# Optimization experiments

Hardware: AMD Instinct MI355X
Metric: run time of the kernel (lower is better)

Reference implementation:

```python
import jax, jax.numpy as jnp
import numpy as np

D_MODEL = 1024
NUM_HEADS = 16
D_K = D_MODEL // NUM_HEADS
THETA = 10000.0
SEQ = 4096
BATCH = 1


def _rope(x, token_positions):
    # x: [b, h, s, d_k]; interleaved even/odd rotation as in the torch module
    kd = jnp.arange(0, D_K, 2, dtype=jnp.float32) / D_K          # [d_k/2]
    angles = token_positions[:, None].astype(jnp.float32) / (THETA ** kd)  # [s, d_k/2]
    cos_pos = jnp.cos(angles)
    sin_pos = jnp.sin(angles)
    x_even = x[..., 0::2]
    x_odd = x[..., 1::2]
    rot_even = x_even * cos_pos - x_odd * sin_pos
    rot_odd = x_even * sin_pos + x_odd * cos_pos
    rot = jnp.stack([rot_even, rot_odd], axis=-1)                # [..., d_k/2, 2]
    return rot.reshape(*x.shape[:-1], D_K)


def setup_inputs() -> dict:
    key = jax.random.key(0)
    k1, k2, k3 = jax.random.split(key, 3)
    std_qkv = np.sqrt(2.0 / (D_MODEL + 3 * D_MODEL))
    std_o = np.sqrt(2.0 / (D_MODEL + D_MODEL))
    x = jax.random.normal(k1, (BATCH, SEQ, D_MODEL), dtype=jnp.float32)
    Wqkv = jax.random.normal(k2, (3 * D_MODEL, D_MODEL), dtype=jnp.float32) * std_qkv
    Wo = jax.random.normal(k3, (D_MODEL, D_MODEL), dtype=jnp.float32) * std_o
    token_positions = jnp.arange(SEQ, dtype=jnp.int32)
    return {"x": x, "Wqkv": Wqkv, "Wo": Wo, "token_positions": token_positions}


def reference(x, Wqkv, Wo, token_positions):
    b, s, _ = x.shape
    qkv = jnp.einsum('bsd,ed->bse', x, Wqkv)                      # [b, s, 3*d_model]
    q, k, v = jnp.split(qkv, 3, axis=-1)

    def to_heads(t):
        return t.reshape(b, s, NUM_HEADS, D_K).transpose(0, 2, 1, 3)  # [b, h, s, d_k]

    q, k, v = to_heads(q), to_heads(k), to_heads(v)
    q = _rope(q, token_positions)
    k = _rope(k, token_positions)

    scores = jnp.einsum('bhqd,bhkd->bhqk', q, k) / jnp.sqrt(jnp.float32(D_K))
    mask = jnp.tril(jnp.ones((s, s), dtype=bool))
    scores = jnp.where(mask, scores, -jnp.inf)
    attn = jax.nn.softmax(scores, axis=-1)
    out = jnp.einsum('bhqk,bhkd->bhqd', attn, v)                  # [b, h, s, d_k]
    out = out.transpose(0, 2, 1, 3).reshape(b, s, D_MODEL)
    return jnp.einsum('bsd,ed->bse', out, Wo)
```

## Files before the change

kernel.cpp:

```cpp
#include <hip/hip_runtime.h>
#include <cstdint>

typedef unsigned short u16;
typedef __attribute__((ext_vector_type(8))) short short8;
typedef __attribute__((ext_vector_type(4))) float float4v;

__device__ __forceinline__ float bf2f(u16 u) {
    union { unsigned int i; float f; } v; v.i = ((unsigned int)u) << 16; return v.f;
}
__device__ __forceinline__ u16 f2bf(float f) {
    union { float f; unsigned int i; } v; v.f = f;
    unsigned int i = v.i;
    i += 0x7fffu + ((i >> 16) & 1u);
    return (u16)(i >> 16);
}
__device__ __forceinline__ unsigned cvt_pk_bf16(float lo, float hi) {
    unsigned r;
    asm("v_cvt_pk_bf16_f32 %0, %1, %2" : "=v"(r) : "v"(lo), "v"(hi));
    return r;
}
__device__ __forceinline__ void gl2lds16(const u16* g, u16* l) {
    __builtin_amdgcn_global_load_lds((const __attribute__((address_space(1))) void*)g,
                                     (__attribute__((address_space(3))) void*)l, 16, 0, 0);
}
__device__ __forceinline__ uint4 cvt8(const float* __restrict__ p) {
    float4 a = *(const float4*)p;
    float4 b = *(const float4*)(p + 4);
    u16 t[8] = {f2bf(a.x), f2bf(a.y), f2bf(a.z), f2bf(a.w),
                f2bf(b.x), f2bf(b.y), f2bf(b.z), f2bf(b.w)};
    return *(const uint4*)t;
}

__global__ void cvt_f32_bf16(const float* __restrict__ src, u16* __restrict__ dst, int n8) {
    int i = blockIdx.x * blockDim.x + threadIdx.x;
    if (i >= n8) return;
    *(uint4*)(dst + (size_t)i * 8) = cvt8(src + (size_t)i * 8);
}

__global__ void zero_f32(float* __restrict__ p, int n4) {
    int i = blockIdx.x * blockDim.x + threadIdx.x;
    if (i >= n4) return;
    float4 z = {0.f, 0.f, 0.f, 0.f};
    *(float4*)(p + (size_t)i * 4) = z;
}

__global__ __launch_bounds__(256) void gemm_bt(const u16* __restrict__ A,
                                               const u16* __restrict__ B,
                                               u16* __restrict__ C,
                                               int M, int N, int K) {
    __shared__ u16 As[128 * 32];
    __shared__ u16 Bs[128 * 32];
    const int tid  = threadIdx.x;
    const int wave = tid >> 6, lane = tid & 63;
    const int lg = lane >> 4, lr = lane & 15;
    const int bm = blockIdx.x * 128, bn = blockIdx.y * 128;
    const int wm = (wave & 1) * 64, wn = (wave >> 1) * 64;
    const int row = tid >> 2, co = (tid & 3) * 8;

    float4v acc[4][4] = {};

    for (int k0 = 0; k0 < K; k0 += 32) {
        gl2lds16(A + (size_t)(bm + row) * K + k0 + co,      As + tid * 8);
        gl2lds16(A + (size_t)(bm + 64 + row) * K + k0 + co, As + (tid + 256) * 8);
        gl2lds16(B + (size_t)(bn + row) * K + k0 + co,      Bs + tid * 8);
        gl2lds16(B + (size_t)(bn + 64 + row) * K + k0 + co, Bs + (tid + 256) * 8);
        __syncthreads();

        short8 af[4], bf[4];
        #pragma unroll
        for (int i = 0; i < 4; ++i)
            af[i] = *(const short8*)(As + (wm + i * 16 + lr) * 32 + lg * 8);
        #pragma unroll
        for (int j = 0; j < 4; ++j)
            bf[j] = *(const short8*)(Bs + (wn + j * 16 + lr) * 32 + lg * 8);
        #pragma unroll
        for (int i = 0; i < 4; ++i)
            #pragma unroll
            for (int j = 0; j < 4; ++j)
                acc[i][j] = __builtin_amdgcn_mfma_f32_16x16x32_bf16(af[i], bf[j], acc[i][j], 0, 0, 0);
        __syncthreads();
    }

    #pragma unroll
    for (int i = 0; i < 4; ++i)
        #pragma unroll
        for (int j = 0; j < 4; ++j)
            #pragma unroll
            for (int r = 0; r < 4; ++r) {
                int rw = bm + wm + i * 16 + lg * 4 + r;
                int cl = bn + wn + j * 16 + lr;
                C[(size_t)rw * N + cl] = f2bf(acc[i][j][r]);
            }
}

__global__ void rope_kernel(u16* __restrict__ qkv, const int* __restrict__ pos, int S) {
    int idx = blockIdx.x * blockDim.x + threadIdx.x;
    int s = idx >> 10;
    if (s >= S) return;
    int p    = idx & 1023;
    int part = p >> 9;
    int wi   = p & 511;
    int head = wi >> 5;
    int i    = wi & 31;
    int col  = part * 1024 + head * 64 + 2 * i;

    u16* ptr = qkv + (size_t)s * 3072 + col;
    ushort2 v = *(const ushort2*)ptr;
    float xe = bf2f(v.x), xo = bf2f(v.y);
    float freq = __expf(-(float)i * 0.2878231366242557f);
    float ang  = (float)pos[s] * freq;
    float sn = sinf(ang), cs = cosf(ang);
    float re = xe * cs - xo * sn;
    float ro = xe * sn + xo * cs;
    if (part == 0) { re *= 0.18033688011112042f; ro *= 0.18033688011112042f; }
    ushort2 o; o.x = f2bf(re); o.y = f2bf(ro);
    *(ushort2*)ptr = o;
}

__global__ __launch_bounds__(256) void transpose_v(const u16* __restrict__ qkv,
                                                   u16* __restrict__ VT) {
    __shared__ u16 T[64 * 65];
    const int h = blockIdx.y, s0 = blockIdx.x * 64;
    const int tid = threadIdx.x;
    #pragma unroll
    for (int i = 0; i < 2; ++i) {
        int seg = i * 256 + tid;
        int r = seg >> 3, c8 = (seg & 7) * 8;
        u16 tmp[8];
        *(uint4*)tmp = *(const uint4*)(qkv + (size_t)(s0 + r) * 3072 + 2048 + h * 64 + c8);
        #pragma unroll
        for (int j = 0; j < 8; ++j) T[r * 65 + c8 + j] = tmp[j];
    }
    __syncthreads();
    #pragma unroll
    for (int i = 0; i < 2; ++i) {
        int seg = i * 256 + tid;
        int d = seg >> 3, s8 = (seg & 7) * 8;
        u16 tmp[8];
        #pragma unroll
        for (int j = 0; j < 8; ++j) tmp[j] = T[(s8 + j) * 65 + d];
        *(uint4*)(VT + (size_t)(h * 64 + d) * 4096 + s0 + s8) = *(const uint4*)tmp;
    }
}

__device__ __forceinline__ void attn_tile(const u16* __restrict__ Ksub,
                                          const u16* __restrict__ Vsub,
                                          u16* __restrict__ Psw,
                                          int tbase, int qrow0, int q_abs,
                                          int lg, int lr, int swz,
                                          const short8 qf[2], float4v o_acc[4], float& rs) {
    float4v sc[4];
    #pragma unroll
    for (int jt = 0; jt < 4; ++jt) {
        float4v a = {};
        #pragma unroll
        for (int kk = 0; kk < 2; ++kk) {
            short8 kf = *(const short8*)(Ksub + (jt * 16 + lr) * 64 + (((kk * 4 + lg) ^ swz) * 8));
            a = __builtin_amdgcn_mfma_f32_16x16x32_bf16(kf, qf[kk], a, 0, 0, 0);
        }
        sc[jt] = a;
    }
    const bool mk = (tbase + 63 > qrow0);
    #pragma unroll
    for (int jt = 0; jt < 4; ++jt) {
        float e[4];
        #pragma unroll
        for (int r = 0; r < 4; ++r) {
            float s = sc[jt][r];
            if (mk && (tbase + jt * 16 + lg * 4 + r > q_abs)) s = -30000.f;
            e[r] = __builtin_amdgcn_exp2f(fminf(s, 86.562f));
        }
        rs += (e[0] + e[1]) + (e[2] + e[3]);
        uint2 w;
        w.x = cvt_pk_bf16(e[0], e[1]);
        w.y = cvt_pk_bf16(e[2], e[3]);
        *(uint2*)(Psw + lr * 72 + jt * 16 + lg * 4) = w;
    }
    short8 pf[2];
    #pragma unroll
    for (int kk = 0; kk < 2; ++kk)
        pf[kk] = *(const short8*)(Psw + lr * 72 + kk * 32 + lg * 8);
    #pragma unroll
    for (int jd = 0; jd < 4; ++jd) {
        float4v a = o_acc[jd];
        #pragma unroll
        for (int kk = 0; kk < 2; ++kk) {
            short8 vf = *(const short8*)(Vsub + (jd * 16 + lr) * 64 + (((kk * 4 + lg) ^ swz) * 8));
            a = __builtin_amdgcn_mfma_f32_16x16x32_bf16(pf[kk], vf, a, 0, 0, 0);
        }
        o_acc[jd] = a;
    }
}

__global__ __launch_bounds__(512) void attn_kernel(const u16* __restrict__ qkv,
                                                   const u16* __restrict__ VT,
                                                   float* __restrict__ acc,
                                                   float* __restrict__ lac) {
    __shared__ u16 Ks[2 * 64 * 64];
    __shared__ u16 Vt[2 * 64 * 64];
    __shared__ u16 Ps[8][16 * 72];

    const int tid  = threadIdx.x;
    const int wave = tid >> 6, lane = tid & 63;
    const int lg = lane >> 4, lr = lane & 15;
    const int h  = blockIdx.y;
    const int z  = blockIdx.z;

    const int srow = tid >> 3;
    const int sg   = tid & 7;
    const int sco  = sg * 8;
    const int sldso = srow * 64 + ((sg ^ (srow & 7)) * 8);
    const int swz = (lr & 7);

    const u16* Kgbase = qkv + (size_t)srow * 3072 + 1024 + h * 64 + sco;
    const u16* Vgbase = VT + (size_t)(h * 64 + srow) * 4096 + sco;

    #pragma unroll 1
    for (int part = 0; part < 2; ++part) {
        const int qt = part ? (31 - (int)blockIdx.x) : (int)blockIdx.x;
        const int qb = qt * 128;
        const int qrow0 = qb + wave * 16;
        const int q_abs = qrow0 + lr;
        const int tmax = qb + 64;
        const int t0s  = z * 64;

        short8 qf[2];
        #pragma unroll
        for (int kk = 0; kk < 2; ++kk)
            qf[kk] = *(const short8*)(qkv + (size_t)(qrow0 + lr) * 3072 + h * 64 + kk * 32 + lg * 8);

        float4v o_acc[4] = {};
        float rs = 0.f;

        uint4 rK0 = *(const uint4*)(Kgbase + (size_t)t0s * 3072);
        uint4 rV0 = *(const uint4*)(Vgbase + t0s);
        const bool pB = (t0s + 128 <= tmax);
        uint4 rK1, rV1;
        if (pB) {
            rK1 = *(const uint4*)(Kgbase + (size_t)(t0s + 128) * 3072);
            rV1 = *(const uint4*)(Vgbase + t0s + 128);
        }
        __syncthreads();
        *(uint4*)(Ks + sldso) = rK0;
        *(uint4*)(Vt + sldso) = rV0;
        if (pB) {
            *(uint4*)(Ks + 4096 + sldso) = rK1;
            *(uint4*)(Vt + 4096 + sldso) = rV1;
        }
        __syncthreads();

        for (int t0 = t0s; t0 <= tmax; t0 += 256) {
            const bool hasB  = (t0 + 128 <= tmax);
            const bool hasN  = (t0 + 256 <= tmax);
            const bool hasNB = (t0 + 384 <= tmax);
            if (hasN) {
                rK0 = *(const uint4*)(Kgbase + (size_t)(t0 + 256) * 3072);
                rV0 = *(const uint4*)(Vgbase + t0 + 256);
            }
            if (hasNB) {
                rK1 = *(const uint4*)(Kgbase + (size_t)(t0 + 384) * 3072);
                rV1 = *(const uint4*)(Vgbase + t0 + 384);
            }

            attn_tile(Ks, Vt, Ps[wave], t0, qrow0, q_abs, lg, lr, swz, qf, o_acc, rs);
            if (hasB)
                attn_tile(Ks + 4096, Vt + 4096, Ps[wave], t0 + 128, qrow0, q_abs,
                          lg, lr, swz, qf, o_acc, rs);

            if (hasN) {
                __syncthreads();
                *(uint4*)(Ks + sldso) = rK0;
                *(uint4*)(Vt + sldso) = rV0;
                if (hasNB) {
                    *(uint4*)(Ks + 4096 + sldso) = rK1;
                    *(uint4*)(Vt + 4096 + sldso) = rV1;
                }
                __syncthreads();
            }
        }

        float t = rs;
        t += __shfl_xor(t, 16, 64);
        t += __shfl_xor(t, 32, 64);
        if (lane < 16)
            atomicAdd(&lac[(size_t)(qrow0 + lr) * 16 + h], t);

        #pragma unroll
        for (int jd = 0; jd < 4; ++jd)
            #pragma unroll
            for (int r = 0; r < 4; ++r) {
                int s = qrow0 + lg * 4 + r;
                int d = jd * 16 + lr;
                atomicAdd(&acc[(size_t)s * 1024 + h * 64 + d], o_acc[jd][r]);
            }
    }
}

__global__ void norm_o(const float* __restrict__ acc, const float* __restrict__ lac,
                       u16* __restrict__ qkv) {
    int i = blockIdx.x * blockDim.x + threadIdx.x;
    if (i >= 4096 * 1024 / 8) return;
    int e0 = i * 8;
    int s = e0 >> 10, c = e0 & 1023, h = c >> 6;
    float inv = 1.0f / lac[(size_t)s * 16 + h];
    float4 a = *(const float4*)(acc + e0);
    float4 b = *(const float4*)(acc + e0 + 4);
    u16 t[8] = {f2bf(a.x * inv), f2bf(a.y * inv), f2bf(a.z * inv), f2bf(a.w * inv),
                f2bf(b.x * inv), f2bf(b.y * inv), f2bf(b.z * inv), f2bf(b.w * inv)};
    *(uint4*)(qkv + (size_t)s * 3072 + c) = *(const uint4*)t;
}

__global__ __launch_bounds__(256) void gemm_oproj(const u16* __restrict__ A,
                                                  const u16* __restrict__ B,
                                                  float* __restrict__ C) {
    __shared__ u16 As[128 * 32];
    __shared__ u16 Bs[128 * 32];
    const int tid  = threadIdx.x;
    const int wave = tid >> 6, lane = tid & 63;
    const int lg = lane >> 4, lr = lane & 15;
    const int bm = blockIdx.x * 128, bn = blockIdx.y * 128;
    const int wm = (wave & 1) * 64, wn = (wave >> 1) * 64;
    const int row = tid >> 2, co = (tid & 3) * 8;

    float4v acc[4][4] = {};

    for (int k0 = 0; k0 < 1024; k0 += 32) {
        gl2lds16(A + (size_t)(bm + row) * 3072 + k0 + co,      As + tid * 8);
        gl2lds16(A + (size_t)(bm + 64 + row) * 3072 + k0 + co, As + (tid + 256) * 8);
        gl2lds16(B + (size_t)(bn + row) * 1024 + k0 + co,      Bs + tid * 8);
        gl2lds16(B + (size_t)(bn + 64 + row) * 1024 + k0 + co, Bs + (tid + 256) * 8);
        __syncthreads();

        short8 af[4], bf[4];
        #pragma unroll
        for (int i = 0; i < 4; ++i)
            af[i] = *(const short8*)(As + (wm + i * 16 + lr) * 32 + lg * 8);
        #pragma unroll
        for (int j = 0; j < 4; ++j)
            bf[j] = *(const short8*)(Bs + (wn + j * 16 + lr) * 32 + lg * 8);
        #pragma unroll
        for (int i = 0; i < 4; ++i)
            #pragma unroll
            for (int j = 0; j < 4; ++j)
                acc[i][j] = __builtin_amdgcn_mfma_f32_16x16x32_bf16(af[i], bf[j], acc[i][j], 0, 0, 0);
        __syncthreads();
    }

    #pragma unroll
    for (int i = 0; i < 4; ++i)
        #pragma unroll
        for (int j = 0; j < 4; ++j)
            #pragma unroll
            for (int r = 0; r < 4; ++r) {
                int rw = bm + wm + i * 16 + lg * 4 + r;
                int cl = bn + wn + j * 16 + lr;
                C[(size_t)rw * 1024 + cl] = acc[i][j][r];
            }
}

__global__ void fill_diag(float* __restrict__ p, size_t n, float mark) {
    size_t i = (size_t)blockIdx.x * blockDim.x + threadIdx.x;
    if (i < n) p[i] = 0.f;
    if (i == 0) p[0] = mark;
}

extern "C" void kernel_launch(void* const* d_in, const int* in_sizes, int n_in,
                              void* d_out, int out_size, void* d_ws, size_t ws_size,
                              hipStream_t stream) {
    int ix = -1, iwq = -1, iwo = -1, ip = -1;
    for (int i = 0; i < n_in; ++i) {
        if      (in_sizes[i] == 4096 * 1024) ix = i;
        else if (in_sizes[i] == 3072 * 1024) iwq = i;
        else if (in_sizes[i] == 1024 * 1024) iwo = i;
        else if (in_sizes[i] == 4096)        ip = i;
    }
    float* out = (float*)d_out;
    const size_t OUT_E = (size_t)4096 * 1024;
    const size_t QKV_E = (size_t)4096 * 3072;
    const size_t NEED  = QKV_E * 2 + (size_t)3072 * 1024 * 2;

    if (ix < 0 || iwq < 0 || iwo < 0 || ip < 0 || out_size != (int)OUT_E) {
        fill_diag<<<(int)((OUT_E + 255) / 256), 256, 0, stream>>>(out, OUT_E, 1000.0f);
        return;
    }
    if (ws_size < NEED) {
        fill_diag<<<(int)((OUT_E + 255) / 256), 256, 0, stream>>>(out, OUT_E, 500.0f);
        return;
    }
    const float* x    = (const float*)d_in[ix];
    const float* Wqkv = (const float*)d_in[iwq];
    const float* Wo   = (const float*)d_in[iwo];
    const int*   pos  = (const int*)d_in[ip];

    u16* qkv   = (u16*)d_ws;
    u16* wq_bf = (u16*)d_ws + QKV_E;
    u16* wo_bf = wq_bf;
    float* lac = (float*)((char*)wq_bf + 2 * 1024 * 1024 + 65536);
    u16* x_bf  = (u16*)d_out;
    u16* VT    = (u16*)d_out + OUT_E;
    float* acc = (float*)d_in[ix];

    cvt_f32_bf16<<<2048, 256, 0, stream>>>(x, x_bf, 4096 * 1024 / 8);
    cvt_f32_bf16<<<1536, 256, 0, stream>>>(Wqkv, wq_bf, 3072 * 1024 / 8);
    gemm_bt<<<dim3(32, 24), 256, 0, stream>>>(x_bf, wq_bf, qkv, 4096, 3072, 1024);
    zero_f32<<<4096, 256, 0, stream>>>(acc, 4096 * 1024 / 4);
    zero_f32<<<16, 256, 0, stream>>>(lac, 4096 * 16 / 4);
    cvt_f32_bf16<<<512, 256, 0, stream>>>(Wo, wo_bf, 1024 * 1024 / 8);
    rope_kernel<<<16384, 256, 0, stream>>>(qkv, pos, 4096);
    transpose_v<<<dim3(64, 16), 256, 0, stream>>>(qkv, VT);
    attn_kernel<<<dim3(16, 16, 2), 512, 0, stream>>>(qkv, VT, acc, lac);
    norm_o<<<2048, 256, 0, stream>>>(acc, lac, qkv);
    gemm_oproj<<<dim3(32, 8), 256, 0, stream>>>(qkv, wo_bf, out);
}
```

Measured before the change: 245.7 us.

## Fuse RoPE into QKV GEMM epilogue, merge prep kernels, split attention KV three ways

Applies RoPE and the Q scaling inside the QKV GEMM epilogue, exchanging the even/odd partner with a lane shuffle, which removes a separate read-modify-write pass over Q and K. The converts and zero-fills are merged into two kernels to reduce launch count. Attention now splits the key range across three z-slices (stride 384, second tile at +192) instead of two, raising block count, and the P scratch row pitch changes from 72 to 80 to alter the LDS bank pattern. This adds per-element sincos work in the GEMM epilogue and relies on the atomic-style accumulation handling a third partial.

```diff
diff --git a/kernel.cpp b/kernel.cpp
--- a/kernel.cpp
+++ b/kernel.cpp
@@ -31,23 +31,35 @@
     return *(const uint4*)t;
 }
 
-__global__ void cvt_f32_bf16(const float* __restrict__ src, u16* __restrict__ dst, int n8) {
+__global__ void cvt_xw(const float* __restrict__ x, const float* __restrict__ wq,
+                       u16* __restrict__ xb, u16* __restrict__ wqb) {
     int i = blockIdx.x * blockDim.x + threadIdx.x;
-    if (i >= n8) return;
-    *(uint4*)(dst + (size_t)i * 8) = cvt8(src + (size_t)i * 8);
-}
-
-__global__ void zero_f32(float* __restrict__ p, int n4) {
+    if (i < 524288) {
+        *(uint4*)(xb + (size_t)i * 8) = cvt8(x + (size_t)i * 8);
+    } else {
+        int j = i - 524288;
+        *(uint4*)(wqb + (size_t)j * 8) = cvt8(wq + (size_t)j * 8);
+    }
+}
+
+__global__ void zero_cvt(float* __restrict__ acc, float* __restrict__ lac,
+                         const float* __restrict__ wo, u16* __restrict__ wob) {
     int i = blockIdx.x * blockDim.x + threadIdx.x;
-    if (i >= n4) return;
     float4 z = {0.f, 0.f, 0.f, 0.f};
-    *(float4*)(p + (size_t)i * 4) = z;
-}
-
-__global__ __launch_bounds__(256) void gemm_bt(const u16* __restrict__ A,
-                                               const u16* __restrict__ B,
-                                               u16* __restrict__ C,
-                                               int M, int N, int K) {
+    if (i < 1048576) {
+        *(float4*)(acc + (size_t)i * 4) = z;
+    } else if (i < 1064960) {
+        *(float4*)(lac + (size_t)(i - 1048576) * 4) = z;
+    } else {
+        int j = i - 1064960;
+        *(uint4*)(wob + (size_t)j * 8) = cvt8(wo + (size_t)j * 8);
+    }
+}
+
+__global__ __launch_bounds__(256) void gemm_qkv(const u16* __restrict__ A,
+                                                const u16* __restrict__ B,
+                                                u16* __restrict__ C,
+                                                const int* __restrict__ pos) {
     __shared__ u16 As[128 * 32];
     __shared__ u16 Bs[128 * 32];
     const int tid  = threadIdx.x;
@@ -59,11 +71,11 @@
 
     float4v acc[4][4] = {};
 
-    for (int k0 = 0; k0 < K; k0 += 32) {
-        gl2lds16(A + (size_t)(bm + row) * K + k0 + co,      As + tid * 8);
-        gl2lds16(A + (size_t)(bm + 64 + row) * K + k0 + co, As + (tid + 256) * 8);
-        gl2lds16(B + (size_t)(bn + row) * K + k0 + co,      Bs + tid * 8);
-        gl2lds16(B + (size_t)(bn + 64 + row) * K + k0 + co, Bs + (tid + 256) * 8);
+    for (int k0 = 0; k0 < 1024; k0 += 32) {
+        gl2lds16(A + (size_t)(bm + row) * 1024 + k0 + co,      As + tid * 8);
+        gl2lds16(A + (size_t)(bm + 64 + row) * 1024 + k0 + co, As + (tid + 256) * 8);
+        gl2lds16(B + (size_t)(bn + row) * 1024 + k0 + co,      Bs + tid * 8);
+        gl2lds16(B + (size_t)(bn + 64 + row) * 1024 + k0 + co, Bs + (tid + 256) * 8);
         __syncthreads();
 
         short8 af[4], bf[4];
@@ -81,40 +93,35 @@
         __syncthreads();
     }
 
+    const int colbase = bn + wn;
+    const bool dorope = colbase < 2048;
+    const float qsc = (colbase < 1024) ? 0.18033688011112042f : 1.0f;
+    float freqs[4];
+    if (dorope) {
+        #pragma unroll
+        for (int j = 0; j < 4; ++j)
+            freqs[j] = __expf(-(float)((j * 16 + lr) >> 1) * 0.2878231366242557f);
+    }
     #pragma unroll
     for (int i = 0; i < 4; ++i)
         #pragma unroll
-        for (int j = 0; j < 4; ++j)
+        for (int r = 0; r < 4; ++r) {
+            const int rw = bm + wm + i * 16 + lg * 4 + r;
+            const float pr = dorope ? (float)pos[rw] : 0.f;
             #pragma unroll
-            for (int r = 0; r < 4; ++r) {
-                int rw = bm + wm + i * 16 + lg * 4 + r;
-                int cl = bn + wn + j * 16 + lr;
-                C[(size_t)rw * N + cl] = f2bf(acc[i][j][r]);
-            }
-}
-
-__global__ void rope_kernel(u16* __restrict__ qkv, const int* __restrict__ pos, int S) {
-    int idx = blockIdx.x * blockDim.x + threadIdx.x;
-    int s = idx >> 10;
-    if (s >= S) return;
-    int p    = idx & 1023;
-    int part = p >> 9;
-    int wi   = p & 511;
-    int head = wi >> 5;
-    int i    = wi & 31;
-    int col  = part * 1024 + head * 64 + 2 * i;
-
-    u16* ptr = qkv + (size_t)s * 3072 + col;
-    ushort2 v = *(const ushort2*)ptr;
-    float xe = bf2f(v.x), xo = bf2f(v.y);
-    float freq = __expf(-(float)i * 0.2878231366242557f);
-    float ang  = (float)pos[s] * freq;
-    float sn = sinf(ang), cs = cosf(ang);
-    float re = xe * cs - xo * sn;
-    float ro = xe * sn + xo * cs;
-    if (part == 0) { re *= 0.18033688011112042f; ro *= 0.18033688011112042f; }
-    ushort2 o; o.x = f2bf(re); o.y = f2bf(ro);
-    *(ushort2*)ptr = o;
+            for (int j = 0; j < 4; ++j) {
+                float v = acc[i][j][r];
+                if (dorope) {
+                    float sn, cs;
+                    __sincosf(pr * freqs[j], &sn, &cs);
+                    float p = __shfl_xor(v, 1);
+                    float rot = (lr & 1) ? (p * sn + v * cs)
+                                         : (v * cs - p * sn);
+                    v = rot * qsc;
+                }
+                C[(size_t)rw * 3072 + colbase + j * 16 + lr] = f2bf(v);
+            }
+        }
 }
 
 __global__ __launch_bounds__(256) void transpose_v(const u16* __restrict__ qkv,
@@ -174,12 +181,12 @@
         uint2 w;
         w.x = cvt_pk_bf16(e[0], e[1]);
         w.y = cvt_pk_bf16(e[2], e[3]);
-        *(uint2*)(Psw + lr * 72 + jt * 16 + lg * 4) = w;
+        *(uint2*)(Psw + lr * 80 + jt * 16 + lg * 4) = w;
     }
     short8 pf[2];
     #pragma unroll
     for (int kk = 0; kk < 2; ++kk)
-        pf[kk] = *(const short8*)(Psw + lr * 72 + kk * 32 + lg * 8);
+        pf[kk] = *(const short8*)(Psw + lr * 80 + kk * 32 + lg * 8);
     #pragma unroll
     for (int jd = 0; jd < 4; ++jd) {
         float4v a = o_acc[jd];
@@ -198,7 +205,7 @@
                                                    float* __restrict__ lac) {
     __shared__ u16 Ks[2 * 64 * 64];
     __shared__ u16 Vt[2 * 64 * 64];
-    __shared__ u16 Ps[8][16 * 72];
+    __shared__ u16 Ps[8][16 * 80];
 
     const int tid  = threadIdx.x;
     const int wave = tid >> 6, lane = tid & 63;
@@ -234,11 +241,11 @@
 
         uint4 rK0 = *(const uint4*)(Kgbase + (size_t)t0s * 3072);
         uint4 rV0 = *(const uint4*)(Vgbase + t0s);
-        const bool pB = (t0s + 128 <= tmax);
+        const bool pB = (t0s + 192 <= tmax);
         uint4 rK1, rV1;
         if (pB) {
-            rK1 = *(const uint4*)(Kgbase + (size_t)(t0s + 128) * 3072);
-            rV1 = *(const uint4*)(Vgbase + t0s + 128);
+            rK1 = *(const uint4*)(Kgbase + (size_t)(t0s + 192) * 3072);
+            rV1 = *(const uint4*)(Vgbase + t0s + 192);
         }
         __syncthreads();
         *(uint4*)(Ks + sldso) = rK0;
@@ -249,22 +256,22 @@
         }
         __syncthreads();
 
-        for (int t0 = t0s; t0 <= tmax; t0 += 256) {
-            const bool hasB  = (t0 + 128 <= tmax);
-            const bool hasN  = (t0 + 256 <= tmax);
-            const bool hasNB = (t0 + 384 <= tmax);
+        for (int t0 = t0s; t0 <= tmax; t0 += 384) {
+            const bool hasB  = (t0 + 192 <= tmax);
+            const bool hasN  = (t0 + 384 <= tmax);
+            const bool hasNB = (t0 + 576 <= tmax);
             if (hasN) {
-                rK0 = *(const uint4*)(Kgbase + (size_t)(t0 + 256) * 3072);
-                rV0 = *(const uint4*)(Vgbase + t0 + 256);
+                rK0 = *(const uint4*)(Kgbase + (size_t)(t0 + 384) * 3072);
+                rV0 = *(const uint4*)(Vgbase + t0 + 384);
             }
             if (hasNB) {
-                rK1 = *(const uint4*)(Kgbase + (size_t)(t0 + 384) * 3072);
-                rV1 = *(const uint4*)(Vgbase + t0 + 384);
+                rK1 = *(const uint4*)(Kgbase + (size_t)(t0 + 576) * 3072);
+                rV1 = *(const uint4*)(Vgbase + t0 + 576);
             }
 
             attn_tile(Ks, Vt, Ps[wave], t0, qrow0, q_abs, lg, lr, swz, qf, o_acc, rs);
             if (hasB)
-                attn_tile(Ks + 4096, Vt + 4096, Ps[wave], t0 + 128, qrow0, q_abs,
+                attn_tile(Ks + 4096, Vt + 4096, Ps[wave], t0 + 192, qrow0, q_abs,
                           lg, lr, swz, qf, o_acc, rs);
 
             if (hasN) {
@@ -400,15 +407,11 @@
     u16* VT    = (u16*)d_out + OUT_E;
     float* acc = (float*)d_in[ix];
 
-    cvt_f32_bf16<<<2048, 256, 0, stream>>>(x, x_bf, 4096 * 1024 / 8);
-    cvt_f32_bf16<<<1536, 256, 0, stream>>>(Wqkv, wq_bf, 3072 * 1024 / 8);
-    gemm_bt<<<dim3(32, 24), 256, 0, stream>>>(x_bf, wq_bf, qkv, 4096, 3072, 1024);
-    zero_f32<<<4096, 256, 0, stream>>>(acc, 4096 * 1024 / 4);
-    zero_f32<<<16, 256, 0, stream>>>(lac, 4096 * 16 / 4);
-    cvt_f32_bf16<<<512, 256, 0, stream>>>(Wo, wo_bf, 1024 * 1024 / 8);
-    rope_kernel<<<16384, 256, 0, stream>>>(qkv, pos, 4096);
+    cvt_xw<<<3584, 256, 0, stream>>>(x, Wqkv, x_bf, wq_bf);
+    gemm_qkv<<<dim3(32, 24), 256, 0, stream>>>(x_bf, wq_bf, qkv, pos);
+    zero_cvt<<<4672, 256, 0, stream>>>(acc, lac, Wo, wo_bf);
     transpose_v<<<dim3(64, 16), 256, 0, stream>>>(qkv, VT);
-    attn_kernel<<<dim3(16, 16, 2), 512, 0, stream>>>(qkv, VT, acc, lac);
+    attn_kernel<<<dim3(16, 16, 3), 512, 0, stream>>>(qkv, VT, acc, lac);
     norm_o<<<2048, 256, 0, stream>>>(acc, lac, qkv);
     gemm_oproj<<<dim3(32, 8), 256, 0, stream>>>(qkv, wo_bf, out);
 }
```

New measurement: 256.5 us. 1.04x slower.
